# Optimization experiments

Hardware: AMD Instinct MI355X
Metric: run time of the kernel (lower is better)

The kernel has to match this reference:

```python
import jax, jax.numpy as jnp
import numpy as np

B, LQ, LKV = 4, 1024, 1024
HID, H, G = 2048, 32, 8
HD = HID // H          # head_dim = 64
HPG = H // G           # heads per group = 4


def setup_inputs() -> dict:
    key = jax.random.key(0)
    ks = jax.random.split(key, 10)
    s = 0.02
    inp = {
        "X": jax.random.normal(ks[0], (B, LQ, HID), jnp.float32),
        "encoder_output": jax.random.normal(ks[1], (B, LKV, HID), jnp.float32),
        # causal mask: True above the diagonal (masked)
        "causal_mask": jnp.triu(jnp.ones((LQ, LKV), bool), 1),
        # padding: last quarter of src positions masked for second half of batch
        "padding_mask": jnp.zeros((B, LKV), bool).at[B // 2:, LKV - LKV // 4:].set(True),
        "Wq": jax.random.normal(ks[2], (HID, HID), jnp.float32) * s,
        "bq": jnp.zeros((HID,), jnp.float32),
        "Wk": jax.random.normal(ks[3], (G * HD, HID), jnp.float32) * s,
        "bk": jnp.zeros((G * HD,), jnp.float32),
        "Wv": jax.random.normal(ks[4], (G * HD, HID), jnp.float32) * s,
        "bv": jnp.zeros((G * HD,), jnp.float32),
        "Wo": jax.random.normal(ks[5], (HID, HID), jnp.float32) * s,
        "bo": jnp.zeros((HID,), jnp.float32),
    }
    return inp


def reference(X, encoder_output, causal_mask, padding_mask,
              Wq, bq, Wk, bk, Wv, bv, Wo, bo):
    b = X.shape[0]
    q = X @ Wq.T + bq                       # (b, Lq, H*HD)
    k = encoder_output @ Wk.T + bk          # (b, Lkv, G*HD)
    v = encoder_output @ Wv.T + bv          # (b, Lkv, G*HD)

    # head index = g * HPG + r  (matches torch expand-then-reshape ordering)
    q = q.reshape(b, LQ, G, HPG, HD).transpose(0, 2, 3, 1, 4)   # (b,G,HPG,Lq,HD)
    k = k.reshape(b, LKV, G, HD).transpose(0, 2, 1, 3)          # (b,G,Lkv,HD)
    v = v.reshape(b, LKV, G, HD).transpose(0, 2, 1, 3)          # (b,G,Lkv,HD)

    scores = jnp.einsum('bgrqd,bgkd->bgrqk', q, k) / jnp.sqrt(jnp.float32(HD))
    scores = jnp.where(causal_mask[None, None, None, :, :], -jnp.inf, scores)
    scores = jnp.where(padding_mask[:, None, None, None, :], -jnp.inf, scores)
    w = jax.nn.softmax(scores, axis=-1)

    out = jnp.einsum('bgrqk,bgkd->bgrqd', w, v)                 # (b,G,HPG,Lq,HD)
    out = out.reshape(b, H, LQ, HD).transpose(0, 2, 1, 3).reshape(b, LQ, HID)
    return out @ Wo.T + bo
```

## Files before the change

kernel.cpp:

```cpp
#include <hip/hip_runtime.h>
#include <hip/hip_bf16.h>
#include <stdint.h>

#define B_    4
#define LQ_   1024
#define LKV_  1024
#define HID_  2048
#define NH_   32
#define NG_   8
#define HD_   64
#define KVD_  (NG_*HD_)

typedef unsigned short u16;
typedef __attribute__((ext_vector_type(8))) short short8;
typedef __attribute__((ext_vector_type(4))) short short4v;
typedef __attribute__((ext_vector_type(4))) float f32x4;

__device__ __forceinline__ u16 f2b(float f) {
  union { float f; uint32_t u; } x; x.f = f;
  uint32_t r = x.u + 0x7fffu + ((x.u >> 16) & 1u);
  return (u16)(r >> 16);
}

__device__ __forceinline__ float fexp2(float x) {
  float r; asm("v_exp_f32 %0, %1" : "=v"(r) : "v"(x)); return r;
}

__device__ __forceinline__ void gload_lds16(const void* gsrc, void* lds) {
  __builtin_amdgcn_global_load_lds(
      (const __attribute__((address_space(1))) unsigned int*)gsrc,
      (__attribute__((address_space(3))) unsigned int*)lds, 16, 0, 0);
}

__device__ __forceinline__ void bar() {
  asm volatile("" ::: "memory");
  __builtin_amdgcn_s_barrier();
  asm volatile("" ::: "memory");
}

struct CastArgs {
  const float* src[6];
  u16* dst[6];
  int cum[7];
};

__global__ __launch_bounds__(256) void cast_all(CastArgs a) {
  const int i = blockIdx.x * 256 + threadIdx.x;
  if (i >= a.cum[6]) return;
  int s = 0;
#pragma unroll
  for (int k = 1; k < 6; ++k) s += (i >= a.cum[k]);
  const int off = i - a.cum[s];
  const float4 v = ((const float4*)a.src[s])[off];
  uint2 o;
  o.x = (uint32_t)f2b(v.x) | ((uint32_t)f2b(v.y) << 16);
  o.y = (uint32_t)f2b(v.z) | ((uint32_t)f2b(v.w) << 16);
  ((uint2*)a.dst[s])[off] = o;
}

template<int MODE>
__global__ __launch_bounds__(256)
void gemm_bt(const u16* __restrict__ A,
             const u16* __restrict__ B0, const float* __restrict__ bias0, void* __restrict__ C0,
             const u16* __restrict__ B1, const float* __restrict__ bias1, void* __restrict__ C1,
             int M, int N, int K) {
  __shared__ u16 As[128 * 64];
  __shared__ u16 Bs[128 * 64];
  const u16* Bm = blockIdx.z ? B1 : B0;
  const float* bias = blockIdx.z ? bias1 : bias0;
  void* C = blockIdx.z ? C1 : C0;

  const int nwg = gridDim.x * gridDim.y;
  const int orig = blockIdx.y * gridDim.x + blockIdx.x;
  const int wg = (orig & 7) * (nwg >> 3) + (orig >> 3);
  const int bx = wg % gridDim.x, by = wg / gridDim.x;

  const int tid = threadIdx.x;
  const int lane = tid & 63, wave = tid >> 6;
  const int l15 = lane & 15, l4 = lane >> 4;
  const int wm = wave >> 1, wn = wave & 1;
  const int m0 = by * 128, n0 = bx * 128;

  f32x4 acc[4][4] = {};

  for (int k0 = 0; k0 < K; k0 += 64) {
#pragma unroll
    for (int j = 0; j < 4; ++j) {
      const int c = (wave * 4 + j) * 64 + lane;
      const int row = c >> 3, cc = (c & 7) * 8;
      gload_lds16(&A[(size_t)(m0 + row) * K + k0 + cc], (void*)&As[c * 8]);
      gload_lds16(&Bm[(size_t)(n0 + row) * K + k0 + cc], (void*)&Bs[c * 8]);
    }
    asm volatile("s_waitcnt vmcnt(0)" ::: "memory");
    __syncthreads();
#pragma unroll
    for (int kk = 0; kk < 2; ++kk) {
      short8 af[4], bf[4];
#pragma unroll
      for (int m = 0; m < 4; ++m)
        af[m] = *(const short8*)&As[(wm * 64 + m * 16 + l15) * 64 + kk * 32 + l4 * 8];
#pragma unroll
      for (int n = 0; n < 4; ++n)
        bf[n] = *(const short8*)&Bs[(wn * 64 + n * 16 + l15) * 64 + kk * 32 + l4 * 8];
#pragma unroll
      for (int m = 0; m < 4; ++m)
#pragma unroll
        for (int n = 0; n < 4; ++n)
          acc[m][n] = __builtin_amdgcn_mfma_f32_16x16x32_bf16(af[m], bf[n], acc[m][n], 0, 0, 0);
    }
    __syncthreads();
  }

  const bool vtstore = (MODE == 2) && (blockIdx.z == 1);
#pragma unroll
  for (int m = 0; m < 4; ++m) {
    const int row0 = m0 + wm * 64 + m * 16 + l4 * 4;
#pragma unroll
    for (int n = 0; n < 4; ++n) {
      const int col = n0 + wn * 64 + n * 16 + l15;
      const float bv = bias[col];
      if (vtstore) {
        const int bb = row0 >> 10, kv = row0 & (LKV_ - 1);
        short4v pk;
#pragma unroll
        for (int r = 0; r < 4; ++r) pk[r] = (short)f2b(acc[m][n][r] + bv);
        *(short4v*)&((u16*)C)[((size_t)col * B_ + bb) * LKV_ + kv] = pk;
      } else {
#pragma unroll
        for (int r = 0; r < 4; ++r) {
          const float v = acc[m][n][r] + bv;
          if (MODE == 1) ((float*)C)[(size_t)(row0 + r) * N + col] = v;
          else           ((u16*)C)[(size_t)(row0 + r) * N + col] = f2b(v);
        }
      }
    }
  }
}

__global__ __launch_bounds__(256)
void attn(const u16* __restrict__ Q, const u16* __restrict__ Kg,
          const u16* __restrict__ Vtg, u16* __restrict__ AO) {
  const int qb = (int)gridDim.x - 1 - (int)blockIdx.x;
  const int h = blockIdx.y, b = blockIdx.z;
  const int g = h >> 2;
  const int tid = threadIdx.x, lane = tid & 63, wave = tid >> 6;
  const int l15 = lane & 15, l4 = lane >> 4;
  const int qw = qb * 64 + wave * 16;

  __shared__ u16 Ks[2][64 * 64];
  __shared__ u16 Vs[2][64 * 64];
  __shared__ u16 Ps[4][16 * 64];

  short8 qf[2];
  {
    const size_t base = ((size_t)(b * LQ_ + qw + l15)) * HID_ + h * HD_ + l4 * 8;
    qf[0] = *(const short8*)&Q[base];
    qf[1] = *(const short8*)&Q[base + 32];
  }

  f32x4 oacc[4] = {};
  float mrun[4], lrun[4];
#pragma unroll
  for (int r = 0; r < 4; ++r) { mrun[r] = -3.0e38f; lrun[r] = 0.f; }

  const int cap = (b >= B_ / 2) ? 12 : 16;
  const int ntile = (qb + 1 < cap) ? (qb + 1) : cap;

  auto stage = [&](int t, int bsel) {
    const int kv0 = t * 64;
    const int c0 = wave * 64 + lane;
#pragma unroll
    for (int j = 0; j < 2; ++j) {
      const int c = j * 256 + c0;
      const int row = c >> 3, ci = c & 7;
      gload_lds16(&Kg[((size_t)(b * LKV_ + kv0 + row)) * KVD_ + g * HD_ + ((ci ^ (row & 7)) << 3)],
                  (void*)&Ks[bsel][c * 8]);
    }
#pragma unroll
    for (int j = 0; j < 2; ++j) {
      const int c = j * 256 + c0;
      const int d = c >> 3, ci = c & 7;
      gload_lds16(&Vtg[((size_t)(g * HD_ + d) * B_ + b) * LKV_ + kv0 + ((ci ^ (d & 7)) << 3)],
                  (void*)&Vs[bsel][c * 8]);
    }
  };

  stage(0, 0);
  for (int t = 0; t < ntile; ++t) {
    const u16* ks = Ks[t & 1];
    const u16* vs = Vs[t & 1];
    if (t + 1 < ntile) {
      stage(t + 1, (t + 1) & 1);
      asm volatile("s_waitcnt vmcnt(4)" ::: "memory");
    } else {
      asm volatile("s_waitcnt vmcnt(0)" ::: "memory");
    }
    __builtin_amdgcn_s_barrier();
    asm volatile("" ::: "memory");

    f32x4 s4[4] = {};
#pragma unroll
    for (int kk = 0; kk < 2; ++kk)
#pragma unroll
      for (int n = 0; n < 4; ++n) {
        const int row = n * 16 + l15;
        const short8 bfr = *(const short8*)&ks[row * 64 + ((kk * 32 + l4 * 8) ^ ((row & 7) << 3))];
        s4[n] = __builtin_amdgcn_mfma_f32_16x16x32_bf16(qf[kk], bfr, s4[n], 0, 0, 0);
      }

    const bool diag = (t == qb);
    float sv[4][4];
#pragma unroll
    for (int n = 0; n < 4; ++n) {
      const int kv = t * 64 + n * 16 + l15;
#pragma unroll
      for (int r = 0; r < 4; ++r) {
        float x = s4[n][r] * 0.1803368843f;
        if (diag && kv > qw + l4 * 4 + r) x = -1.0e30f;
        sv[n][r] = x;
      }
    }

    float mnew[4], resc[4], psum[4];
#pragma unroll
    for (int r = 0; r < 4; ++r) {
      float mx = fmaxf(fmaxf(sv[0][r], sv[1][r]), fmaxf(sv[2][r], sv[3][r]));
      mx = fmaxf(mx, __shfl_xor(mx, 1));
      mx = fmaxf(mx, __shfl_xor(mx, 2));
      mx = fmaxf(mx, __shfl_xor(mx, 4));
      mx = fmaxf(mx, __shfl_xor(mx, 8));
      mnew[r] = fmaxf(mrun[r], mx);
      resc[r] = fexp2(mrun[r] - mnew[r]);
      mrun[r] = mnew[r];
      lrun[r] *= resc[r];
      psum[r] = 0.f;
    }
#pragma unroll
    for (int n = 0; n < 4; ++n)
#pragma unroll
      for (int r = 0; r < 4; ++r) {
        oacc[n][r] *= resc[r];
        const float p = fexp2(sv[n][r] - mnew[r]);
        psum[r] += p;
        const int prow = l4 * 4 + r, pcol = n * 16 + l15;
        Ps[wave][prow * 64 + (pcol ^ ((prow & 7) << 3))] = f2b(p);
      }
#pragma unroll
    for (int r = 0; r < 4; ++r) {
      float su = psum[r];
      su += __shfl_xor(su, 1);
      su += __shfl_xor(su, 2);
      su += __shfl_xor(su, 4);
      su += __shfl_xor(su, 8);
      lrun[r] += su;
    }

#pragma unroll
    for (int kk = 0; kk < 2; ++kk) {
      const short8 pa = *(const short8*)&Ps[wave][l15 * 64 + ((kk * 32 + l4 * 8) ^ ((l15 & 7) << 3))];
#pragma unroll
      for (int n = 0; n < 4; ++n) {
        const int row = n * 16 + l15;
        const short8 vb = *(const short8*)&vs[row * 64 + ((kk * 32 + l4 * 8) ^ ((row & 7) << 3))];
        oacc[n] = __builtin_amdgcn_mfma_f32_16x16x32_bf16(pa, vb, oacc[n], 0, 0, 0);
      }
    }
    bar();
  }

  float rinv[4];
#pragma unroll
  for (int r = 0; r < 4; ++r) rinv[r] = 1.f / lrun[r];
#pragma unroll
  for (int n = 0; n < 4; ++n)
#pragma unroll
    for (int r = 0; r < 4; ++r)
      AO[((size_t)(b * LQ_ + qw + l4 * 4 + r)) * HID_ + h * HD_ + n * 16 + l15] =
          f2b(oacc[n][r] * rinv[r]);
}

extern "C" void kernel_launch(void* const* d_in, const int* in_sizes, int n_in,
                              void* d_out, int out_size, void* d_ws, size_t ws_size,
                              hipStream_t stream) {
  const float* X  = (const float*)d_in[0];
  const float* E  = (const float*)d_in[1];
  const float* Wq = (const float*)d_in[4];
  const float* bq = (const float*)d_in[5];
  const float* Wk = (const float*)d_in[6];
  const float* bk = (const float*)d_in[7];
  const float* Wv = (const float*)d_in[8];
  const float* bv = (const float*)d_in[9];
  const float* Wo = (const float*)d_in[10];
  const float* bo = (const float*)d_in[11];
  float* out = (float*)d_out;

  char* w = (char*)d_ws;
  u16* Xb  = (u16*)(w);
  u16* Eb  = (u16*)(w + 16777216);
  u16* Wqb = (u16*)(w + 33554432);
  u16* Wkb = (u16*)(w + 41943040);
  u16* Wvb = (u16*)(w + 44040192);
  u16* Wob = (u16*)(w + 46137344);
  u16* Qb  = (u16*)(w + 54525952);
  u16* Kb  = (u16*)(w + 71303168);
  u16* Vtb = (u16*)(w + 75497472);
  u16* AOb = Xb;

  CastArgs ca;
  ca.src[0] = X;  ca.dst[0] = Xb;
  ca.src[1] = E;  ca.dst[1] = Eb;
  ca.src[2] = Wq; ca.dst[2] = Wqb;
  ca.src[3] = Wk; ca.dst[3] = Wkb;
  ca.src[4] = Wv; ca.dst[4] = Wvb;
  ca.src[5] = Wo; ca.dst[5] = Wob;
  const int n4s[6] = {2097152, 2097152, 1048576, 262144, 262144, 1048576};
  ca.cum[0] = 0;
  for (int i = 0; i < 6; ++i) ca.cum[i + 1] = ca.cum[i] + n4s[i];
  hipLaunchKernelGGL(cast_all, dim3((ca.cum[6] + 255) / 256), dim3(256), 0, stream, ca);

  const int M = B_ * LQ_;

  hipLaunchKernelGGL((gemm_bt<0>), dim3(HID_ / 128, M / 128, 1), dim3(256), 0, stream,
                     Xb, Wqb, bq, (void*)Qb, Wqb, bq, (void*)Qb, M, HID_, HID_);
  hipLaunchKernelGGL((gemm_bt<2>), dim3(KVD_ / 128, M / 128, 2), dim3(256), 0, stream,
                     Eb, Wkb, bk, (void*)Kb, Wvb, bv, (void*)Vtb, M, KVD_, HID_);
  hipLaunchKernelGGL(attn, dim3(LQ_ / 64, NH_, B_), dim3(256), 0, stream, Qb, Kb, Vtb, AOb);
  hipLaunchKernelGGL((gemm_bt<1>), dim3(HID_ / 128, M / 128, 1), dim3(256), 0, stream,
                     AOb, Wob, bo, (void*)out, Wob, bo, (void*)out, M, HID_, HID_);
}
```

Measured before the change: 400.9 us.

## Merge QKV GEMMs, share KV tiles across GQA heads, use 32x32 MFMA in attention

The Q, K and V projections now run in one 768-block launch with a fixed XCD-aware tile remap, and the output projection gets its own kernel with a similar remap. Attention now launches one 512-thread block per KV group, so all four heads of a group share one staged K/V tile, which cuts redundant K/V loads. It also moves to 32x32x16 MFMA with register-resident P, passing P between lanes with a shuffle instead of an LDS round trip. The cost is more registers per thread and larger blocks, which may lower occupancy in attention.

```diff
diff --git a/kernel.cpp b/kernel.cpp
--- a/kernel.cpp
+++ b/kernel.cpp
@@ -15,6 +15,7 @@
 typedef __attribute__((ext_vector_type(8))) short short8;
 typedef __attribute__((ext_vector_type(4))) short short4v;
 typedef __attribute__((ext_vector_type(4))) float f32x4;
+typedef __attribute__((ext_vector_type(16))) float f32x16;
 
 __device__ __forceinline__ u16 f2b(float f) {
   union { float f; uint32_t u; } x; x.f = f;
@@ -30,12 +31,6 @@
   __builtin_amdgcn_global_load_lds(
       (const __attribute__((address_space(1))) unsigned int*)gsrc,
       (__attribute__((address_space(3))) unsigned int*)lds, 16, 0, 0);
-}
-
-__device__ __forceinline__ void bar() {
-  asm volatile("" ::: "memory");
-  __builtin_amdgcn_s_barrier();
-  asm volatile("" ::: "memory");
 }
 
 struct CastArgs {
@@ -58,22 +53,31 @@
   ((uint2*)a.dst[s])[off] = o;
 }
 
-template<int MODE>
 __global__ __launch_bounds__(256)
-void gemm_bt(const u16* __restrict__ A,
-             const u16* __restrict__ B0, const float* __restrict__ bias0, void* __restrict__ C0,
-             const u16* __restrict__ B1, const float* __restrict__ bias1, void* __restrict__ C1,
-             int M, int N, int K) {
+void qkv_gemm(const u16* __restrict__ Xb, const u16* __restrict__ Eb,
+              const u16* __restrict__ Wq, const float* __restrict__ bq, u16* __restrict__ Qb,
+              const u16* __restrict__ Wk, const float* __restrict__ bk, u16* __restrict__ Kb,
+              const u16* __restrict__ Wv, const float* __restrict__ bv, u16* __restrict__ Vtb) {
   __shared__ u16 As[128 * 64];
   __shared__ u16 Bs[128 * 64];
-  const u16* Bm = blockIdx.z ? B1 : B0;
-  const float* bias = blockIdx.z ? bias1 : bias0;
-  void* C = blockIdx.z ? C1 : C0;
-
-  const int nwg = gridDim.x * gridDim.y;
-  const int orig = blockIdx.y * gridDim.x + blockIdx.x;
-  const int wg = (orig & 7) * (nwg >> 3) + (orig >> 3);
-  const int bx = wg % gridDim.x, by = wg / gridDim.x;
+
+  const int orig = blockIdx.x;
+  const int wg = (orig & 7) * 96 + (orig >> 3);
+
+  const u16* A; const u16* Bw; const float* bias; u16* C;
+  int N, bx, by, vt = 0;
+  if (wg < 512) {
+    A = Xb; Bw = Wq; bias = bq; C = Qb; N = HID_;
+    bx = wg & 15; by = ((wg >> 6) << 2) | ((wg >> 4) & 3);
+  } else if (wg < 640) {
+    const int l = wg - 512;
+    A = Eb; Bw = Wk; bias = bk; C = Kb; N = KVD_;
+    bx = l & 3; by = l >> 2;
+  } else {
+    const int l = wg - 640;
+    A = Eb; Bw = Wv; bias = bv; C = Vtb; N = KVD_;
+    bx = l & 3; by = l >> 2; vt = 1;
+  }
 
   const int tid = threadIdx.x;
   const int lane = tid & 63, wave = tid >> 6;
@@ -83,13 +87,13 @@
 
   f32x4 acc[4][4] = {};
 
-  for (int k0 = 0; k0 < K; k0 += 64) {
+  for (int k0 = 0; k0 < HID_; k0 += 64) {
 #pragma unroll
     for (int j = 0; j < 4; ++j) {
       const int c = (wave * 4 + j) * 64 + lane;
       const int row = c >> 3, cc = (c & 7) * 8;
-      gload_lds16(&A[(size_t)(m0 + row) * K + k0 + cc], (void*)&As[c * 8]);
-      gload_lds16(&Bm[(size_t)(n0 + row) * K + k0 + cc], (void*)&Bs[c * 8]);
+      gload_lds16(&A[(size_t)(m0 + row) * HID_ + k0 + cc], (void*)&As[c * 8]);
+      gload_lds16(&Bw[(size_t)(n0 + row) * HID_ + k0 + cc], (void*)&Bs[c * 8]);
     }
     asm volatile("s_waitcnt vmcnt(0)" ::: "memory");
     __syncthreads();
@@ -111,78 +115,119 @@
     __syncthreads();
   }
 
-  const bool vtstore = (MODE == 2) && (blockIdx.z == 1);
 #pragma unroll
   for (int m = 0; m < 4; ++m) {
     const int row0 = m0 + wm * 64 + m * 16 + l4 * 4;
 #pragma unroll
     for (int n = 0; n < 4; ++n) {
       const int col = n0 + wn * 64 + n * 16 + l15;
-      const float bv = bias[col];
-      if (vtstore) {
+      const float bvv = bias[col];
+      if (vt) {
         const int bb = row0 >> 10, kv = row0 & (LKV_ - 1);
         short4v pk;
 #pragma unroll
-        for (int r = 0; r < 4; ++r) pk[r] = (short)f2b(acc[m][n][r] + bv);
-        *(short4v*)&((u16*)C)[((size_t)col * B_ + bb) * LKV_ + kv] = pk;
+        for (int r = 0; r < 4; ++r) pk[r] = (short)f2b(acc[m][n][r] + bvv);
+        *(short4v*)&C[((size_t)col * B_ + bb) * LKV_ + kv] = pk;
       } else {
 #pragma unroll
-        for (int r = 0; r < 4; ++r) {
-          const float v = acc[m][n][r] + bv;
-          if (MODE == 1) ((float*)C)[(size_t)(row0 + r) * N + col] = v;
-          else           ((u16*)C)[(size_t)(row0 + r) * N + col] = f2b(v);
-        }
+        for (int r = 0; r < 4; ++r)
+          C[(size_t)(row0 + r) * N + col] = f2b(acc[m][n][r] + bvv);
       }
     }
   }
 }
 
 __global__ __launch_bounds__(256)
+void o_gemm(const u16* __restrict__ A, const u16* __restrict__ Bw,
+            const float* __restrict__ bias, float* __restrict__ C) {
+  __shared__ u16 As[128 * 64];
+  __shared__ u16 Bs[128 * 64];
+  const int orig = blockIdx.x;
+  const int wg = (orig & 7) * 64 + (orig >> 3);
+  const int bx = wg & 15, by = ((wg >> 6) << 2) | ((wg >> 4) & 3);
+
+  const int tid = threadIdx.x;
+  const int lane = tid & 63, wave = tid >> 6;
+  const int l15 = lane & 15, l4 = lane >> 4;
+  const int wm = wave >> 1, wn = wave & 1;
+  const int m0 = by * 128, n0 = bx * 128;
+
+  f32x4 acc[4][4] = {};
+  for (int k0 = 0; k0 < HID_; k0 += 64) {
+#pragma unroll
+    for (int j = 0; j < 4; ++j) {
+      const int c = (wave * 4 + j) * 64 + lane;
+      const int row = c >> 3, cc = (c & 7) * 8;
+      gload_lds16(&A[(size_t)(m0 + row) * HID_ + k0 + cc], (void*)&As[c * 8]);
+      gload_lds16(&Bw[(size_t)(n0 + row) * HID_ + k0 + cc], (void*)&Bs[c * 8]);
+    }
+    asm volatile("s_waitcnt vmcnt(0)" ::: "memory");
+    __syncthreads();
+#pragma unroll
+    for (int kk = 0; kk < 2; ++kk) {
+      short8 af[4], bf[4];
+#pragma unroll
+      for (int m = 0; m < 4; ++m)
+        af[m] = *(const short8*)&As[(wm * 64 + m * 16 + l15) * 64 + kk * 32 + l4 * 8];
+#pragma unroll
+      for (int n = 0; n < 4; ++n)
+        bf[n] = *(const short8*)&Bs[(wn * 64 + n * 16 + l15) * 64 + kk * 32 + l4 * 8];
+#pragma unroll
+      for (int m = 0; m < 4; ++m)
+#pragma unroll
+        for (int n = 0; n < 4; ++n)
+          acc[m][n] = __builtin_amdgcn_mfma_f32_16x16x32_bf16(af[m], bf[n], acc[m][n], 0, 0, 0);
+    }
+    __syncthreads();
+  }
+#pragma unroll
+  for (int m = 0; m < 4; ++m) {
+    const int row0 = m0 + wm * 64 + m * 16 + l4 * 4;
+#pragma unroll
+    for (int n = 0; n < 4; ++n) {
+      const int col = n0 + wn * 64 + n * 16 + l15;
+      const float bvv = bias[col];
+#pragma unroll
+      for (int r = 0; r < 4; ++r)
+        C[(size_t)(row0 + r) * HID_ + col] = acc[m][n][r] + bvv;
+    }
+  }
+}
+
+__global__ __launch_bounds__(512)
 void attn(const u16* __restrict__ Q, const u16* __restrict__ Kg,
           const u16* __restrict__ Vtg, u16* __restrict__ AO) {
-  const int qb = (int)gridDim.x - 1 - (int)blockIdx.x;
-  const int h = blockIdx.y, b = blockIdx.z;
-  const int g = h >> 2;
+  const int qb = 15 - (int)blockIdx.x;
+  const int g = blockIdx.y, b = blockIdx.z;
   const int tid = threadIdx.x, lane = tid & 63, wave = tid >> 6;
-  const int l15 = lane & 15, l4 = lane >> 4;
-  const int qw = qb * 64 + wave * 16;
+  const int l31 = lane & 31, hi = lane >> 5, hi4 = hi * 4;
+  const int h = g * 4 + (wave >> 1);
+  const int qrow = qb * 64 + (wave & 1) * 32 + l31;
 
   __shared__ u16 Ks[2][64 * 64];
   __shared__ u16 Vs[2][64 * 64];
-  __shared__ u16 Ps[4][16 * 64];
-
-  short8 qf[2];
+
+  short8 qf[4];
   {
-    const size_t base = ((size_t)(b * LQ_ + qw + l15)) * HID_ + h * HD_ + l4 * 8;
-    qf[0] = *(const short8*)&Q[base];
-    qf[1] = *(const short8*)&Q[base + 32];
-  }
-
-  f32x4 oacc[4] = {};
-  float mrun[4], lrun[4];
-#pragma unroll
-  for (int r = 0; r < 4; ++r) { mrun[r] = -3.0e38f; lrun[r] = 0.f; }
+    const size_t base = ((size_t)(b * LQ_ + qrow)) * HID_ + h * HD_ + hi * 8;
+#pragma unroll
+    for (int kk = 0; kk < 4; ++kk) qf[kk] = *(const short8*)&Q[base + kk * 16];
+  }
+
+  f32x16 o0 = {}, o1 = {};
+  float mrun = -3.0e38f, lrun = 0.f;
 
   const int cap = (b >= B_ / 2) ? 12 : 16;
   const int ntile = (qb + 1 < cap) ? (qb + 1) : cap;
 
   auto stage = [&](int t, int bsel) {
     const int kv0 = t * 64;
-    const int c0 = wave * 64 + lane;
-#pragma unroll
-    for (int j = 0; j < 2; ++j) {
-      const int c = j * 256 + c0;
-      const int row = c >> 3, ci = c & 7;
-      gload_lds16(&Kg[((size_t)(b * LKV_ + kv0 + row)) * KVD_ + g * HD_ + ((ci ^ (row & 7)) << 3)],
-                  (void*)&Ks[bsel][c * 8]);
-    }
-#pragma unroll
-    for (int j = 0; j < 2; ++j) {
-      const int c = j * 256 + c0;
-      const int d = c >> 3, ci = c & 7;
-      gload_lds16(&Vtg[((size_t)(g * HD_ + d) * B_ + b) * LKV_ + kv0 + ((ci ^ (d & 7)) << 3)],
-                  (void*)&Vs[bsel][c * 8]);
-    }
+    const int c = wave * 64 + lane;
+    const int rowk = c >> 3, cik = c & 7;
+    gload_lds16(&Kg[((size_t)(b * LKV_ + kv0 + rowk)) * KVD_ + g * HD_ + (((cik ^ (rowk & 7))) << 3)],
+                (void*)&Ks[bsel][c * 8]);
+    gload_lds16(&Vtg[((size_t)(g * HD_ + rowk) * B_ + b) * LKV_ + kv0 + (((cik ^ (rowk & 7))) << 3)],
+                (void*)&Vs[bsel][c * 8]);
   };
 
   stage(0, 0);
@@ -191,92 +236,99 @@
     const u16* vs = Vs[t & 1];
     if (t + 1 < ntile) {
       stage(t + 1, (t + 1) & 1);
-      asm volatile("s_waitcnt vmcnt(4)" ::: "memory");
+      asm volatile("s_waitcnt vmcnt(2)" ::: "memory");
     } else {
       asm volatile("s_waitcnt vmcnt(0)" ::: "memory");
     }
     __builtin_amdgcn_s_barrier();
     asm volatile("" ::: "memory");
 
-    f32x4 s4[4] = {};
-#pragma unroll
-    for (int kk = 0; kk < 2; ++kk)
-#pragma unroll
-      for (int n = 0; n < 4; ++n) {
-        const int row = n * 16 + l15;
-        const short8 bfr = *(const short8*)&ks[row * 64 + ((kk * 32 + l4 * 8) ^ ((row & 7) << 3))];
-        s4[n] = __builtin_amdgcn_mfma_f32_16x16x32_bf16(qf[kk], bfr, s4[n], 0, 0, 0);
+    f32x16 s0 = {}, s1 = {};
+#pragma unroll
+    for (int kk = 0; kk < 4; ++kk) {
+      const int ci = kk * 2 + hi;
+      const int r0 = l31, r1 = 32 + l31;
+      const short8 k0 = *(const short8*)&ks[r0 * 64 + ((ci ^ (r0 & 7)) << 3)];
+      const short8 k1 = *(const short8*)&ks[r1 * 64 + ((ci ^ (r1 & 7)) << 3)];
+      s0 = __builtin_amdgcn_mfma_f32_32x32x16_bf16(k0, qf[kk], s0, 0, 0, 0);
+      s1 = __builtin_amdgcn_mfma_f32_32x32x16_bf16(k1, qf[kk], s1, 0, 0, 0);
+    }
+
+    const bool diag = (t == qb);
+    const float SC = 0.180336881f;
+    float mx = -1.0e30f;
+#pragma unroll
+    for (int r = 0; r < 16; ++r) {
+      const int kvr = (r & 3) + 8 * (r >> 2) + hi4;
+      float x0 = s0[r] * SC, x1 = s1[r] * SC;
+      if (diag) {
+        if (t * 64 + kvr > qrow)      x0 = -1.0e30f;
+        if (t * 64 + 32 + kvr > qrow) x1 = -1.0e30f;
       }
-
-    const bool diag = (t == qb);
-    float sv[4][4];
-#pragma unroll
-    for (int n = 0; n < 4; ++n) {
-      const int kv = t * 64 + n * 16 + l15;
-#pragma unroll
-      for (int r = 0; r < 4; ++r) {
-        float x = s4[n][r] * 0.1803368843f;
-        if (diag && kv > qw + l4 * 4 + r) x = -1.0e30f;
-        sv[n][r] = x;
+      s0[r] = x0; s1[r] = x1;
+      mx = fmaxf(mx, fmaxf(x0, x1));
+    }
+    mx = fmaxf(mx, __shfl_xor(mx, 32));
+    const float mnew = fmaxf(mrun, mx);
+    const float resc = fexp2(mrun - mnew);
+    mrun = mnew;
+
+    float sm = 0.f;
+#pragma unroll
+    for (int r = 0; r < 16; ++r) {
+      const float p0 = fexp2(s0[r] - mnew);
+      const float p1 = fexp2(s1[r] - mnew);
+      s0[r] = p0; s1[r] = p1;
+      sm += p0 + p1;
+    }
+    lrun = lrun * resc + (sm + __shfl_xor(sm, 32));
+
+#pragma unroll
+    for (int r = 0; r < 16; ++r) { o0[r] *= resc; o1[r] *= resc; }
+
+    auto pvblock = [&](const f32x16& pv, int nk) {
+#pragma unroll
+      for (int rb = 0; rb < 2; ++rb) {
+        const int b0 = rb * 8;
+        const uint32_t P1 = ((uint32_t)f2b(pv[b0 + 1]) << 16) | f2b(pv[b0 + 0]);
+        const uint32_t P2 = ((uint32_t)f2b(pv[b0 + 3]) << 16) | f2b(pv[b0 + 2]);
+        const uint32_t P3 = ((uint32_t)f2b(pv[b0 + 5]) << 16) | f2b(pv[b0 + 4]);
+        const uint32_t P4 = ((uint32_t)f2b(pv[b0 + 7]) << 16) | f2b(pv[b0 + 6]);
+        const uint32_t t1 = (uint32_t)__shfl_xor((int)(hi ? P1 : P3), 32);
+        const uint32_t t2 = (uint32_t)__shfl_xor((int)(hi ? P2 : P4), 32);
+        union { uint32_t u[4]; short8 s8; } pb;
+        pb.u[0] = hi ? t1 : P1;
+        pb.u[1] = hi ? t2 : P2;
+        pb.u[2] = hi ? P3 : t1;
+        pb.u[3] = hi ? P4 : t2;
+        const int ci = (nk * 2 + rb) * 2 + hi;
+        const int r0 = l31, r1 = 32 + l31;
+        const short8 v0 = *(const short8*)&vs[r0 * 64 + ((ci ^ (r0 & 7)) << 3)];
+        const short8 v1 = *(const short8*)&vs[r1 * 64 + ((ci ^ (r1 & 7)) << 3)];
+        o0 = __builtin_amdgcn_mfma_f32_32x32x16_bf16(v0, pb.s8, o0, 0, 0, 0);
+        o1 = __builtin_amdgcn_mfma_f32_32x32x16_bf16(v1, pb.s8, o1, 0, 0, 0);
       }
-    }
-
-    float mnew[4], resc[4], psum[4];
-#pragma unroll
-    for (int r = 0; r < 4; ++r) {
-      float mx = fmaxf(fmaxf(sv[0][r], sv[1][r]), fmaxf(sv[2][r], sv[3][r]));
-      mx = fmaxf(mx, __shfl_xor(mx, 1));
-      mx = fmaxf(mx, __shfl_xor(mx, 2));
-      mx = fmaxf(mx, __shfl_xor(mx, 4));
-      mx = fmaxf(mx, __shfl_xor(mx, 8));
-      mnew[r] = fmaxf(mrun[r], mx);
-      resc[r] = fexp2(mrun[r] - mnew[r]);
-      mrun[r] = mnew[r];
-      lrun[r] *= resc[r];
-      psum[r] = 0.f;
-    }
-#pragma unroll
-    for (int n = 0; n < 4; ++n)
-#pragma unroll
-      for (int r = 0; r < 4; ++r) {
-        oacc[n][r] *= resc[r];
-        const float p = fexp2(sv[n][r] - mnew[r]);
-        psum[r] += p;
-        const int prow = l4 * 4 + r, pcol = n * 16 + l15;
-        Ps[wave][prow * 64 + (pcol ^ ((prow & 7) << 3))] = f2b(p);
-      }
-#pragma unroll
-    for (int r = 0; r < 4; ++r) {
-      float su = psum[r];
-      su += __shfl_xor(su, 1);
-      su += __shfl_xor(su, 2);
-      su += __shfl_xor(su, 4);
-      su += __shfl_xor(su, 8);
-      lrun[r] += su;
-    }
-
-#pragma unroll
-    for (int kk = 0; kk < 2; ++kk) {
-      const short8 pa = *(const short8*)&Ps[wave][l15 * 64 + ((kk * 32 + l4 * 8) ^ ((l15 & 7) << 3))];
-#pragma unroll
-      for (int n = 0; n < 4; ++n) {
-        const int row = n * 16 + l15;
-        const short8 vb = *(const short8*)&vs[row * 64 + ((kk * 32 + l4 * 8) ^ ((row & 7) << 3))];
-        oacc[n] = __builtin_amdgcn_mfma_f32_16x16x32_bf16(pa, vb, oacc[n], 0, 0, 0);
-      }
-    }
-    bar();
-  }
-
-  float rinv[4];
-#pragma unroll
-  for (int r = 0; r < 4; ++r) rinv[r] = 1.f / lrun[r];
-#pragma unroll
-  for (int n = 0; n < 4; ++n)
-#pragma unroll
-    for (int r = 0; r < 4; ++r)
-      AO[((size_t)(b * LQ_ + qw + l4 * 4 + r)) * HID_ + h * HD_ + n * 16 + l15] =
-          f2b(oacc[n][r] * rinv[r]);
+    };
+    pvblock(s0, 0);
+    pvblock(s1, 1);
+
+    __builtin_amdgcn_s_barrier();
+    asm volatile("" ::: "memory");
+  }
+
+  const float rinv = 1.f / lrun;
+  const size_t base = ((size_t)(b * LQ_ + qrow)) * HID_ + h * HD_;
+#pragma unroll
+  for (int rq = 0; rq < 4; ++rq) {
+    short4v p0, p1;
+#pragma unroll
+    for (int j = 0; j < 4; ++j) {
+      p0[j] = (short)f2b(o0[rq * 4 + j] * rinv);
+      p1[j] = (short)f2b(o1[rq * 4 + j] * rinv);
+    }
+    *(short4v*)&AO[base + rq * 8 + hi4] = p0;
+    *(short4v*)&AO[base + 32 + rq * 8 + hi4] = p1;
+  }
 }
 
 extern "C" void kernel_launch(void* const* d_in, const int* in_sizes, int n_in,
@@ -318,13 +370,8 @@
   for (int i = 0; i < 6; ++i) ca.cum[i + 1] = ca.cum[i] + n4s[i];
   hipLaunchKernelGGL(cast_all, dim3((ca.cum[6] + 255) / 256), dim3(256), 0, stream, ca);
 
-  const int M = B_ * LQ_;
-
-  hipLaunchKernelGGL((gemm_bt<0>), dim3(HID_ / 128, M / 128, 1), dim3(256), 0, stream,
-                     Xb, Wqb, bq, (void*)Qb, Wqb, bq, (void*)Qb, M, HID_, HID_);
-  hipLaunchKernelGGL((gemm_bt<2>), dim3(KVD_ / 128, M / 128, 2), dim3(256), 0, stream,
-                     Eb, Wkb, bk, (void*)Kb, Wvb, bv, (void*)Vtb, M, KVD_, HID_);
-  hipLaunchKernelGGL(attn, dim3(LQ_ / 64, NH_, B_), dim3(256), 0, stream, Qb, Kb, Vtb, AOb);
-  hipLaunchKernelGGL((gemm_bt<1>), dim3(HID_ / 128, M / 128, 1), dim3(256), 0, stream,
-                     AOb, Wob, bo, (void*)out, Wob, bo, (void*)out, M, HID_, HID_);
-}
+  hipLaunchKernelGGL(qkv_gemm, dim3(768), dim3(256), 0, stream,
+                     Xb, Eb, Wqb, bq, Qb, Wkb, bk, Kb, Wvb, bv, Vtb);
+  hipLaunchKernelGGL(attn, dim3(16, NG_, B_), dim3(512), 0, stream, Qb, Kb, Vtb, AOb);
+  hipLaunchKernelGGL(o_gemm, dim3(512), dim3(256), 0, stream, AOb, Wob, bo, out);
+}
```

Measured after the change: 383.9 us. 1.04x faster.
